# Kernel tuning notes

Hardware: AMD Instinct MI355X
Metric: run time of the kernel (lower is better)

Reference implementation:

```python
import jax, jax.numpy as jnp
import numpy as np
from functools import partial

S = 4096      # total tokens (single-request prefill)
H = 32        # indexer heads
D = 128       # indexer head dim (power of 2 for Hadamard)
R = 64        # rope head dim
QLR = 1536    # q_lora_rank
HID = 2048    # hidden size
TOPK = 2048   # index_topk
EPS = 1e-6
NEG = -1e30


def fwht(x):
    """Fast Walsh-Hadamard transform over last dim, scaled by d**-0.5."""
    d = x.shape[-1]
    orig = x.shape
    x = x.reshape(-1, d)
    h = 1
    while h < d:
        x = x.reshape(-1, d // (2 * h), 2, h)
        a, b = x[:, :, 0, :], x[:, :, 1, :]
        x = jnp.stack([a + b, a - b], axis=2).reshape(-1, d)
        h *= 2
    return (x * (d ** -0.5)).reshape(orig)


def apply_rope_interleaved(x, cos, sin):
    # non-neox (interleaved pairs): (x0,x1) -> (x0*c - x1*s, x0*s + x1*c)
    xe, xo = x[..., 0::2], x[..., 1::2]
    return jnp.stack([xe * cos - xo * sin, xe * sin + xo * cos], axis=-1).reshape(x.shape)


def setup_inputs() -> dict:
    key = jax.random.key(0)
    ks = jax.random.split(key, 8)
    hidden_states = jax.random.normal(ks[0], (S, HID), dtype=jnp.float32)
    q_lora = jax.random.normal(ks[1], (S, QLR), dtype=jnp.float32)
    positions = jnp.arange(S, dtype=jnp.int32)
    Wq = jax.random.normal(ks[2], (QLR, H * D), dtype=jnp.float32) * 0.02
    Wk = jax.random.normal(ks[3], (HID, D), dtype=jnp.float32) * 0.02
    k_gamma = jnp.ones((D,), dtype=jnp.float32)
    k_beta = jnp.zeros((D,), dtype=jnp.float32)
    Wp = jax.random.normal(ks[4], (HID, H), dtype=jnp.float32) * 0.02
    return {"hidden_states": hidden_states, "q_lora": q_lora, "positions": positions,
            "Wq": Wq, "Wk": Wk, "k_gamma": k_gamma, "k_beta": k_beta, "Wp": Wp}


def _indexer_logits(hidden_states, q_lora, Wq, Wk, k_gamma, k_beta, Wp, positions):
    # q projection: [S, QLR] @ [QLR, H*D] -> [S, H, D]
    q = (q_lora @ Wq).reshape(S, H, D)
    # k projection + layernorm: [S, D]
    k = hidden_states @ Wk
    mu = jnp.mean(k, axis=-1, keepdims=True)
    var = jnp.mean(jnp.square(k - mu), axis=-1, keepdims=True)
    k = (k - mu) * jax.lax.rsqrt(var + EPS) * k_gamma + k_beta
    # RoPE on first R dims (interleaved / non-neox style)
    half = R // 2
    inv_freq = 1.0 / (10000.0 ** (jnp.arange(half, dtype=jnp.float32) * 2.0 / R))
    ang = positions.astype(jnp.float32)[:, None] * inv_freq          # [S, half]
    cos, sin = jnp.cos(ang), jnp.sin(ang)
    q = q.at[..., :R].set(apply_rope_interleaved(q[..., :R], cos[:, None, :], sin[:, None, :]))
    k = k.at[..., :R].set(apply_rope_interleaved(k[..., :R], cos, sin))
    # Hadamard activation rotation
    q = fwht(q)
    k = fwht(k)
    # per-head gate: weights_proj(x) * n_heads^-0.5 * q_scale(=1) * softmax_scale
    w = (hidden_states @ Wp) * (H ** -0.5) * (D ** -0.5)             # [S, H]
    # logits[t, s] = sum_h w[t, h] * relu(q[t, h] . k[s]); scan over heads
    k_t = k.T                                                         # [D, S]
    def head_step(acc, inp):
        qh, wh = inp                                                  # [S, D], [S]
        return acc + wh[:, None] * jax.nn.relu(qh @ k_t), None
    logits, _ = jax.lax.scan(head_step, jnp.zeros((S, S), jnp.float32),
                             (q.transpose(1, 0, 2), w.T))
    # causal mask (ks=0, ke=t+1 per token for single-request prefill)
    idx = jnp.arange(S)
    logits = jnp.where(idx[None, :] <= idx[:, None], logits, NEG)
    return logits


def reference(hidden_states, q_lora, positions, Wq, Wk, k_gamma, k_beta, Wp):
    logits = _indexer_logits(hidden_states, q_lora, Wq, Wk, k_gamma, k_beta, Wp, positions)
    vals, topk_idx = jax.lax.top_k(logits, TOPK)                      # [S, TOPK]
    topk_idx = jnp.where(vals > NEG * 0.5, topk_idx, -1).astype(jnp.int32)
    return logits, topk_idx
```

## Files before the change

kernel.cpp:

```cpp
#include <hip/hip_runtime.h>
#include <hip/hip_bf16.h>
#include <math.h>

#define S 4096
#define H 32
#define D 128
#define QLR 1536
#define HID 2048
#define TOPK_N 2048
#define NEGF (-1e30f)
#define KW_N 160

typedef __attribute__((ext_vector_type(8))) short bf16x8;
typedef __attribute__((ext_vector_type(4))) float f32x4;

__device__ __forceinline__ void async_copy16(const void* g, void* l) {
    __builtin_amdgcn_global_load_lds(
        (const __attribute__((address_space(1))) unsigned int*)g,
        (__attribute__((address_space(3))) unsigned int*)l,
        16, 0, 0);
}

__device__ __forceinline__ unsigned short bf16bits(float f) {
    __hip_bfloat16 h = __float2bfloat16(f);
    return *(unsigned short*)&h;
}

__device__ __forceinline__ float bits2f(unsigned short u) {
    unsigned v = ((unsigned)u) << 16;
    return __uint_as_float(v);
}

__global__ __launch_bounds__(256) void cast_bf16_kernel(
    const float* __restrict__ in, __hip_bfloat16* __restrict__ out, int n4)
{
    int i = blockIdx.x * blockDim.x + threadIdx.x;
    if (i < n4) {
        float4 v = ((const float4*)in)[i];
        ushort4 pack;
        pack.x = bf16bits(v.x);
        pack.y = bf16bits(v.y);
        pack.z = bf16bits(v.z);
        pack.w = bf16bits(v.w);
        *(ushort4*)(out + (size_t)i * 4) = pack;
    }
}

__global__ __launch_bounds__(256) void zero_f32(float* __restrict__ p, int n)
{
    int i = blockIdx.x * blockDim.x + threadIdx.x;
    if (i < n) p[i] = 0.0f;
}

__global__ __launch_bounds__(256) void transpose_cast_kernel(
    const float* __restrict__ in, __hip_bfloat16* __restrict__ out)
{
    __shared__ float sm[32][33];
    const int nb = blockIdx.x;
    const int kb = blockIdx.y;
    const int t = threadIdx.x;
    const int j = t & 31, i0 = t >> 5;
#pragma unroll
    for (int u = 0; u < 4; ++u) {
        int i = i0 + u * 8;
        sm[i][j] = in[(size_t)(kb * 32 + i) * 4096 + nb * 32 + j];
    }
    __syncthreads();
#pragma unroll
    for (int u = 0; u < 4; ++u) {
        int i = i0 + u * 8;
        out[(size_t)(nb * 32 + i) * 1536 + kb * 32 + j] = __float2bfloat16(sm[j][i]);
    }
}

__global__ __launch_bounds__(256) void build_wkpT(
    const float* __restrict__ Wk, const float* __restrict__ Wp,
    __hip_bfloat16* __restrict__ WkpT)
{
    int g = blockIdx.x * blockDim.x + threadIdx.x;
    if (g >= KW_N * HID) return;
    int n = g / HID, k = g % HID;
    float v = (n < 128) ? Wk[(size_t)k * 128 + n]
                        : Wp[(size_t)k * 32 + (n - 128)] * 0.015625f;
    WkpT[g] = __float2bfloat16(v);
}

__device__ __forceinline__ void kw_stage(
    const short* __restrict__ hb, const short* __restrict__ WkpT,
    int mt, int koff, int rhi, int e, int wave, short* bufA, short* bufB)
{
#pragma unroll
    for (int it = 0; it < 4; ++it) {
        int r = it * 16 + rhi;
        async_copy16(hb + (size_t)(mt * 64 + r) * HID + koff + e * 8,
                     (void*)(bufA + it * 2048 + wave * 512));
    }
#pragma unroll
    for (int it = 0; it < 10; ++it) {
        int r = it * 16 + rhi;
        async_copy16(WkpT + (size_t)r * HID + koff + e * 8,
                     (void*)(bufB + it * 2048 + wave * 512));
    }
}

__global__ __launch_bounds__(256) void kw_mfma(
    const short* __restrict__ hb,
    const short* __restrict__ WkpT,
    float* __restrict__ kf32,
    float* __restrict__ wbuf)
{
    const int mt = blockIdx.x;
    const int kbase = blockIdx.y * 512;
    const int tid = threadIdx.x;
    const int wave = tid >> 6, lane = tid & 63, grp = lane >> 4, lm = lane & 15;
    __shared__ short As[2][64 * 128];
    __shared__ short Bs[2][KW_N * 128];

    const int rhi = tid >> 4;
    const int e = (tid & 15) ^ rhi;

    kw_stage(hb, WkpT, mt, kbase, rhi, e, wave, As[0], Bs[0]);

    f32x4 acc[10] = {};
    int cur = 0;
    for (int kc = 0; kc < 4; ++kc) {
        __syncthreads();
        if (kc < 3)
            kw_stage(hb, WkpT, mt, kbase + (kc + 1) * 128, rhi, e, wave,
                     As[cur ^ 1], Bs[cur ^ 1]);
#pragma unroll
        for (int k4 = 0; k4 < 4; ++k4) {
            int ch = ((k4 << 2) + grp) ^ lm;
            bf16x8 a = *(const bf16x8*)(As[cur] + (wave * 16 + lm) * 128 + ch * 8);
#pragma unroll
            for (int n = 0; n < 10; ++n) {
                bf16x8 b = *(const bf16x8*)(Bs[cur] + (n * 16 + lm) * 128 + ch * 8);
                acc[n] = __builtin_amdgcn_mfma_f32_16x16x32_bf16(a, b, acc[n], 0, 0, 0);
            }
        }
        cur ^= 1;
    }

#pragma unroll
    for (int n = 0; n < 10; ++n) {
#pragma unroll
        for (int r = 0; r < 4; ++r) {
            int row = mt * 64 + wave * 16 + grp * 4 + r;
            int col = n * 16 + lm;
            if (n < 8) atomicAdd(&kf32[(size_t)row * 128 + col], acc[n][r]);
            else       atomicAdd(&wbuf[(size_t)row * 32 + (col - 128)], acc[n][r]);
        }
    }
}

__device__ __forceinline__ void gemm_stage(
    const short* __restrict__ Ag, const short* __restrict__ Bg,
    int row0, int col0, int K, int kc, int tid, int wave, short* as, short* bs)
{
#pragma unroll
    for (int is = 0; is < 2; ++is) {
        int r = is * 64 + (tid >> 2);
        async_copy16(Ag + (size_t)(row0 + r) * K + kc + (tid & 3) * 8,
                     (void*)(as + is * 2048 + wave * 512));
        async_copy16(Bg + (size_t)(col0 + r) * K + kc + (tid & 3) * 8,
                     (void*)(bs + is * 2048 + wave * 512));
    }
}

__global__ __launch_bounds__(256, 2) void gemm_bf16_bt(
    const __hip_bfloat16* __restrict__ A, const __hip_bfloat16* __restrict__ BT,
    __hip_bfloat16* __restrict__ C, int M, int N, int K)
{
    __shared__ short As[2][128 * 32];
    __shared__ short Bs[2][128 * 32];
    const int tid = threadIdx.x;
    const int wave = tid >> 6, lane = tid & 63, grp = lane >> 4, lm = lane & 15;
    const int row0 = blockIdx.y * 128, col0 = blockIdx.x * 128;
    const short* Ag = (const short*)A;
    const short* Bg = (const short*)BT;

    f32x4 acc[2][8] = {};

    gemm_stage(Ag, Bg, row0, col0, K, 0, tid, wave, As[0], Bs[0]);
    int cur = 0;
    for (int kc = 0; kc < K; kc += 32) {
        __syncthreads();
        if (kc + 32 < K)
            gemm_stage(Ag, Bg, row0, col0, K, kc + 32, tid, wave,
                       As[cur ^ 1], Bs[cur ^ 1]);
        bf16x8 a0 = *(const bf16x8*)(As[cur] + (wave * 32 + lm) * 32 + grp * 8);
        bf16x8 a1 = *(const bf16x8*)(As[cur] + (wave * 32 + 16 + lm) * 32 + grp * 8);
#pragma unroll
        for (int c = 0; c < 8; ++c) {
            bf16x8 b = *(const bf16x8*)(Bs[cur] + (c * 16 + lm) * 32 + grp * 8);
            acc[0][c] = __builtin_amdgcn_mfma_f32_16x16x32_bf16(a0, b, acc[0][c], 0, 0, 0);
            acc[1][c] = __builtin_amdgcn_mfma_f32_16x16x32_bf16(a1, b, acc[1][c], 0, 0, 0);
        }
        cur ^= 1;
    }
#pragma unroll
    for (int t = 0; t < 2; ++t)
#pragma unroll
        for (int c = 0; c < 8; ++c)
#pragma unroll
            for (int r = 0; r < 4; ++r) {
                int rr = row0 + wave * 32 + t * 16 + grp * 4 + r;
                int cc = col0 + c * 16 + lm;
                C[(size_t)rr * N + cc] = __float2bfloat16(acc[t][c][r]);
            }
}

__global__ void sincos_table_kernel(const int* __restrict__ positions,
                                    float* __restrict__ cosT, float* __restrict__ sinT)
{
    int g = blockIdx.x * blockDim.x + threadIdx.x;
    if (g >= S * 32) return;
    int s = g >> 5;
    int p = g & 31;
    double inv = pow(10000.0, -((double)(2 * p)) / 64.0);
    double ang = (double)positions[s] * inv;
    cosT[g] = (float)cos(ang);
    sinT[g] = (float)sin(ang);
}

__global__ __launch_bounds__(256) void post_wave(
    const void* __restrict__ in, int in_bf16, __hip_bfloat16* __restrict__ outb,
    const float* __restrict__ cosT, const float* __restrict__ sinT,
    const float* __restrict__ gamma, const float* __restrict__ beta,
    int heads, int do_ln, int nrows)
{
    const int row = blockIdx.x * 4 + (threadIdx.x >> 6);
    if (row >= nrows) return;
    const int l = threadIdx.x & 63;
    const int srow = row / heads;

    float a, b;
    if (in_bf16) {
        unsigned pr = ((const unsigned*)in)[(size_t)row * 64 + l];
        a = bits2f((unsigned short)(pr & 0xffff));
        b = bits2f((unsigned short)(pr >> 16));
    } else {
        float2 v = ((const float2*)in)[(size_t)row * 64 + l];
        a = v.x; b = v.y;
    }

    if (do_ln) {
        float s = a + b;
#pragma unroll
        for (int o = 1; o < 64; o <<= 1) s += __shfl_xor(s, o);
        float mu = s * (1.0f / 128.0f);
        float da = a - mu, db = b - mu;
        float sq = da * da + db * db;
#pragma unroll
        for (int o = 1; o < 64; o <<= 1) sq += __shfl_xor(sq, o);
        float rs = rsqrtf(sq * (1.0f / 128.0f) + 1e-6f);
        float2 g = ((const float2*)gamma)[l];
        float2 bt = ((const float2*)beta)[l];
        a = da * rs * g.x + bt.x;
        b = db * rs * g.y + bt.y;
    }

    if (l < 32) {
        float c = cosT[(size_t)srow * 32 + l];
        float sn = sinT[(size_t)srow * 32 + l];
        float xe = a, xo = b;
        a = xe * c - xo * sn;
        b = xe * sn + xo * c;
    }

    {
        float na = a + b, nb = a - b;
        a = na; b = nb;
    }
#pragma unroll
    for (int m = 1; m < 64; m <<= 1) {
        float pa = __shfl_xor(a, m);
        float pb = __shfl_xor(b, m);
        if (l & m) { a = pa - a; b = pb - b; }
        else       { a = a + pa; b = b + pb; }
    }

    const float sc = 0.08838834764831845f;
    unsigned outp = (unsigned)bf16bits(a * sc) | ((unsigned)bf16bits(b * sc) << 16);
    ((unsigned*)outb)[(size_t)row * 64 + l] = outp;
}

__global__ __launch_bounds__(256, 3) void logits_mfma(
    const short* __restrict__ qb,
    const short* __restrict__ kb,
    const float* __restrict__ w,
    float* __restrict__ out)
{
    const int bx = blockIdx.x;
    const int by = blockIdx.y;
    const int row0 = by * 64, col0 = bx * 128;
    const int tid = threadIdx.x;

    if (2 * bx > by) {
        const float4 n4 = make_float4(NEGF, NEGF, NEGF, NEGF);
        int c = (tid & 31) * 4;
        for (int r = tid >> 5; r < 64; r += 8)
            *(float4*)&out[(size_t)(row0 + r) * S + col0 + c] = n4;
        return;
    }

    __shared__ short BsAs[128 * 128];
    __shared__ float Ws[64 * 33];

    const int wave = tid >> 6, lane = tid & 63, grp = lane >> 4, lm = lane & 15;
    const int wr = wave >> 1, wc = wave & 1;
    const int rhi = tid >> 4;
    const int e = (tid & 15) ^ rhi;

#pragma unroll
    for (int it = 0; it < 8; ++it) {
        int r = it * 16 + rhi;
        async_copy16(kb + (size_t)(col0 + r) * D + e * 8,
                     (void*)(BsAs + it * 2048 + wave * 512));
    }
    for (int i = tid; i < 64 * 32; i += 256) {
        int r = i >> 5, h = i & 31;
        Ws[r * 33 + h] = w[(size_t)row0 * H + i];
    }
    __syncthreads();

    bf16x8 bfrag[4][4];
#pragma unroll
    for (int c = 0; c < 4; ++c)
#pragma unroll
        for (int kc = 0; kc < 4; ++kc)
            bfrag[c][kc] = *(const bf16x8*)(
                BsAs + (wc * 64 + c * 16 + lm) * 128 + (((kc << 2) + grp) ^ lm) * 8);
    __syncthreads();

    short* As0 = BsAs;
    short* As1 = BsAs + 64 * 128;

#pragma unroll
    for (int it = 0; it < 4; ++it) {
        int r = it * 16 + rhi;
        async_copy16(qb + (size_t)(row0 + r) * (H * D) + e * 8,
                     (void*)(As0 + it * 2048 + wave * 512));
    }

    f32x4 accP[2][4] = {};

    for (int h = 0; h < H; ++h) {
        __syncthreads();
        short* Acur  = (h & 1) ? As1 : As0;
        short* Anext = (h & 1) ? As0 : As1;
        if (h + 1 < H) {
#pragma unroll
            for (int it = 0; it < 4; ++it) {
                int r = it * 16 + rhi;
                async_copy16(qb + (size_t)(row0 + r) * (H * D) + (h + 1) * D + e * 8,
                             (void*)(Anext + it * 2048 + wave * 512));
            }
        }
        float wv[2][4];
#pragma unroll
        for (int t = 0; t < 2; ++t)
#pragma unroll
            for (int r = 0; r < 4; ++r)
                wv[t][r] = Ws[(wr * 32 + t * 16 + grp * 4 + r) * 33 + h];

        f32x4 accH[2][4] = {};
        __builtin_amdgcn_s_setprio(1);
#pragma unroll
        for (int kc = 0; kc < 4; ++kc) {
            int ch = ((kc << 2) + grp) ^ lm;
            bf16x8 a0 = *(const bf16x8*)(Acur + (wr * 32 + lm) * 128 + ch * 8);
            bf16x8 a1 = *(const bf16x8*)(Acur + (wr * 32 + 16 + lm) * 128 + ch * 8);
#pragma unroll
            for (int c = 0; c < 4; ++c) {
                accH[0][c] = __builtin_amdgcn_mfma_f32_16x16x32_bf16(a0, bfrag[c][kc], accH[0][c], 0, 0, 0);
                accH[1][c] = __builtin_amdgcn_mfma_f32_16x16x32_bf16(a1, bfrag[c][kc], accH[1][c], 0, 0, 0);
            }
        }
        __builtin_amdgcn_s_setprio(0);
#pragma unroll
        for (int t = 0; t < 2; ++t)
#pragma unroll
            for (int c = 0; c < 4; ++c)
#pragma unroll
                for (int r = 0; r < 4; ++r)
                    accP[t][c][r] += wv[t][r] * fmaxf(accH[t][c][r], 0.0f);
    }

#pragma unroll
    for (int t = 0; t < 2; ++t)
#pragma unroll
        for (int c = 0; c < 4; ++c)
#pragma unroll
            for (int r = 0; r < 4; ++r) {
                int rr = row0 + wr * 32 + t * 16 + grp * 4 + r;
                int cc = col0 + wc * 64 + c * 16 + lm;
                out[(size_t)rr * S + cc] = (cc <= rr) ? accP[t][c][r] : NEGF;
            }
}

__device__ __forceinline__ unsigned mono32(float f)
{
    unsigned u = __float_as_uint(f);
    return (u & 0x80000000u) ? ~u : (u | 0x80000000u);
}

__global__ __launch_bounds__(256) void topk_select(
    const float* __restrict__ logits, float* __restrict__ out_idx)
{
    const int row = blockIdx.x;
    const int tid = threadIdx.x;
    const int valid = row + 1;
    float* orow = out_idx + (size_t)row * TOPK_N;

    if (valid <= TOPK_N) {
        for (int p = tid; p < TOPK_N; p += 256)
            orow[p] = (p < valid) ? (float)p : -1.0f;
        return;
    }

    __shared__ float vals[S];
    __shared__ unsigned hist[2048];
    __shared__ unsigned chunk[256];
    __shared__ unsigned long long sh_prefix;
    __shared__ int sh_rem;
    __shared__ unsigned sh_cnt;

    const float* lr = logits + (size_t)row * S;
    for (int j = tid; j < valid; j += 256) vals[j] = lr[j];
    if (tid == 0) { sh_prefix = 0ull; sh_rem = TOPK_N; sh_cnt = 0u; }
    __syncthreads();

    for (int rnd = 0; rnd < 4; ++rnd) {
        const int shift = 33 - 11 * rnd;
        for (int i = tid; i < 2048; i += 256) hist[i] = 0u;
        __syncthreads();
        const unsigned long long pref = sh_prefix;
        const int rem = sh_rem;
        const int hs = shift + 11;
        for (int j = tid; j < valid; j += 256) {
            unsigned long long key = (((unsigned long long)mono32(vals[j])) << 12)
                                   | (unsigned)(4095 - j);
            if ((key >> hs) == (pref >> hs))
                atomicAdd(&hist[(unsigned)(key >> shift) & 2047u], 1u);
        }
        __syncthreads();
        unsigned csum = 0;
#pragma unroll
        for (int d = 0; d < 8; ++d) csum += hist[tid * 8 + d];
        chunk[tid] = csum;
        __syncthreads();
        for (int off = 1; off < 256; off <<= 1) {
            unsigned v = (tid + off < 256) ? chunk[tid + off] : 0u;
            __syncthreads();
            chunk[tid] += v;
            __syncthreads();
        }
        unsigned A = (tid < 255) ? chunk[tid + 1] : 0u;
        for (int dd = 7; dd >= 0; --dd) {
            unsigned c = hist[tid * 8 + dd];
            if (c && A < (unsigned)rem && (unsigned)rem <= A + c) {
                sh_prefix = pref | ((unsigned long long)(tid * 8 + dd) << shift);
                sh_rem = rem - (int)A;
            }
            A += c;
        }
        __syncthreads();
    }

    const unsigned long long Kstar = sh_prefix;
    for (int j = tid; j < valid; j += 256) {
        unsigned long long key = (((unsigned long long)mono32(vals[j])) << 12)
                               | (unsigned)(4095 - j);
        if (key >= Kstar) {
            unsigned p = atomicAdd(&sh_cnt, 1u);
            orow[p] = (float)j;
        }
    }
}

extern "C" void kernel_launch(void* const* d_in, const int* in_sizes, int n_in,
                              void* d_out, int out_size, void* d_ws, size_t ws_size,
                              hipStream_t stream)
{
    const float* hidden    = (const float*)d_in[0];
    const float* q_lora    = (const float*)d_in[1];
    const int*   positions = (const int*)d_in[2];
    const float* Wq        = (const float*)d_in[3];
    const float* Wk        = (const float*)d_in[4];
    const float* k_gamma   = (const float*)d_in[5];
    const float* k_beta    = (const float*)d_in[6];
    const float* Wp        = (const float*)d_in[7];

    char* ws = (char*)d_ws;
    size_t off = 0;
    __hip_bfloat16* qb16 = (__hip_bfloat16*)(ws + off); off += (size_t)S * H * D * 2;
    __hip_bfloat16* qlb  = (__hip_bfloat16*)(ws + off); off += (size_t)S * QLR * 2;
    __hip_bfloat16* WqT  = (__hip_bfloat16*)(ws + off); off += (size_t)(H * D) * QLR * 2;
    __hip_bfloat16* hb   = (__hip_bfloat16*)(ws + off); off += (size_t)S * HID * 2;
    __hip_bfloat16* WkpT = (__hip_bfloat16*)(ws + off); off += (size_t)KW_N * HID * 2;
    float* kf32 = (float*)(ws + off); off += (size_t)S * D * 4;
    __hip_bfloat16* kb16 = (__hip_bfloat16*)(ws + off); off += (size_t)S * D * 2;
    float* wbuf = (float*)(ws + off); off += (size_t)S * H * 4;
    float* cosT = (float*)(ws + off); off += (size_t)S * 32 * 4;
    float* sinT = (float*)(ws + off); off += (size_t)S * 32 * 4;

    float* out_logits = (float*)d_out;
    float* out_idx = out_logits + (size_t)S * S;

    cast_bf16_kernel<<<(S * QLR / 4 + 255) / 256, 256, 0, stream>>>(q_lora, qlb, S * QLR / 4);
    transpose_cast_kernel<<<dim3((H * D) / 32, QLR / 32), 256, 0, stream>>>(Wq, WqT);

    gemm_bf16_bt<<<dim3((H * D) / 128, S / 128), 256, 0, stream>>>(
        qlb, WqT, qb16, S, H * D, QLR);

    cast_bf16_kernel<<<(S * HID / 4 + 255) / 256, 256, 0, stream>>>(hidden, hb, S * HID / 4);
    build_wkpT<<<(KW_N * HID + 255) / 256, 256, 0, stream>>>(Wk, Wp, WkpT);
    zero_f32<<<(S * D + 255) / 256, 256, 0, stream>>>(kf32, S * D);
    zero_f32<<<(S * H + 255) / 256, 256, 0, stream>>>(wbuf, S * H);
    kw_mfma<<<dim3(S / 64, 4), 256, 0, stream>>>(
        (const short*)hb, (const short*)WkpT, kf32, wbuf);

    sincos_table_kernel<<<(S * 32) / 256, 256, 0, stream>>>(positions, cosT, sinT);

    post_wave<<<(S + 3) / 4, 256, 0, stream>>>(
        kf32, 0, kb16, cosT, sinT, k_gamma, k_beta, 1, 1, S);
    post_wave<<<(S * H + 3) / 4, 256, 0, stream>>>(
        qb16, 1, qb16, cosT, sinT, nullptr, nullptr, H, 0, S * H);

    logits_mfma<<<dim3(S / 128, S / 64), 256, 0, stream>>>(
        (const short*)qb16, (const short*)kb16, wbuf, out_logits);

    topk_select<<<S, 256, 0, stream>>>(out_logits, out_idx);
}
```

Before: 437.9 us.

## Load Q fragments directly to registers in logits kernel, widen GEMM K-tile

The logits kernel no longer stages per-head Q tiles through LDS with barriers. Each wave now loads its Q fragments straight from global memory into registers, double-buffered across heads, so the per-head __syncthreads disappears. Occupancy is lowered to 2 blocks per CU to make room for the extra registers. The projection GEMM moves from a 32 to a 64-wide K tile with an XOR-swizzled LDS layout, and the sincos table uses float math instead of double, which may change numerics slightly.

```diff
diff --git a/kernel.cpp b/kernel.cpp
--- a/kernel.cpp
+++ b/kernel.cpp
@@ -153,17 +153,20 @@
     }
 }
 
-__device__ __forceinline__ void gemm_stage(
+__device__ __forceinline__ void gemm_stage64(
     const short* __restrict__ Ag, const short* __restrict__ Bg,
-    int row0, int col0, int K, int kc, int tid, int wave, short* as, short* bs)
-{
-#pragma unroll
-    for (int is = 0; is < 2; ++is) {
-        int r = is * 64 + (tid >> 2);
-        async_copy16(Ag + (size_t)(row0 + r) * K + kc + (tid & 3) * 8,
-                     (void*)(as + is * 2048 + wave * 512));
-        async_copy16(Bg + (size_t)(col0 + r) * K + kc + (tid & 3) * 8,
-                     (void*)(bs + is * 2048 + wave * 512));
+    int row0, int col0, int K, int kc, int tid, short* as, short* bs)
+{
+    const int w = tid >> 6, lane = tid & 63;
+    const int rsub = lane >> 3;
+    const int c = (lane & 7) ^ rsub;
+#pragma unroll
+    for (int i = 0; i < 4; ++i) {
+        int r = w * 32 + i * 8 + rsub;
+        async_copy16(Ag + (size_t)(row0 + r) * K + kc + c * 8,
+                     (void*)(as + (w * 32 + i * 8) * 64));
+        async_copy16(Bg + (size_t)(col0 + r) * K + kc + c * 8,
+                     (void*)(bs + (w * 32 + i * 8) * 64));
     }
 }
 
@@ -171,8 +174,8 @@
     const __hip_bfloat16* __restrict__ A, const __hip_bfloat16* __restrict__ BT,
     __hip_bfloat16* __restrict__ C, int M, int N, int K)
 {
-    __shared__ short As[2][128 * 32];
-    __shared__ short Bs[2][128 * 32];
+    __shared__ short As[2][128 * 64];
+    __shared__ short Bs[2][128 * 64];
     const int tid = threadIdx.x;
     const int wave = tid >> 6, lane = tid & 63, grp = lane >> 4, lm = lane & 15;
     const int row0 = blockIdx.y * 128, col0 = blockIdx.x * 128;
@@ -181,20 +184,24 @@
 
     f32x4 acc[2][8] = {};
 
-    gemm_stage(Ag, Bg, row0, col0, K, 0, tid, wave, As[0], Bs[0]);
+    gemm_stage64(Ag, Bg, row0, col0, K, 0, tid, As[0], Bs[0]);
     int cur = 0;
-    for (int kc = 0; kc < K; kc += 32) {
+    for (int kc = 0; kc < K; kc += 64) {
         __syncthreads();
-        if (kc + 32 < K)
-            gemm_stage(Ag, Bg, row0, col0, K, kc + 32, tid, wave,
-                       As[cur ^ 1], Bs[cur ^ 1]);
-        bf16x8 a0 = *(const bf16x8*)(As[cur] + (wave * 32 + lm) * 32 + grp * 8);
-        bf16x8 a1 = *(const bf16x8*)(As[cur] + (wave * 32 + 16 + lm) * 32 + grp * 8);
-#pragma unroll
-        for (int c = 0; c < 8; ++c) {
-            bf16x8 b = *(const bf16x8*)(Bs[cur] + (c * 16 + lm) * 32 + grp * 8);
-            acc[0][c] = __builtin_amdgcn_mfma_f32_16x16x32_bf16(a0, b, acc[0][c], 0, 0, 0);
-            acc[1][c] = __builtin_amdgcn_mfma_f32_16x16x32_bf16(a1, b, acc[1][c], 0, 0, 0);
+        if (kc + 64 < K)
+            gemm_stage64(Ag, Bg, row0, col0, K, kc + 64, tid,
+                         As[cur ^ 1], Bs[cur ^ 1]);
+#pragma unroll
+        for (int k2 = 0; k2 < 2; ++k2) {
+            int pos = ((k2 << 2) + grp) ^ (lm & 7);
+            bf16x8 a0 = *(const bf16x8*)(As[cur] + (wave * 32 + lm) * 64 + pos * 8);
+            bf16x8 a1 = *(const bf16x8*)(As[cur] + (wave * 32 + 16 + lm) * 64 + pos * 8);
+#pragma unroll
+            for (int c = 0; c < 8; ++c) {
+                bf16x8 b = *(const bf16x8*)(Bs[cur] + (c * 16 + lm) * 64 + pos * 8);
+                acc[0][c] = __builtin_amdgcn_mfma_f32_16x16x32_bf16(a0, b, acc[0][c], 0, 0, 0);
+                acc[1][c] = __builtin_amdgcn_mfma_f32_16x16x32_bf16(a1, b, acc[1][c], 0, 0, 0);
+            }
         }
         cur ^= 1;
     }
@@ -217,10 +224,12 @@
     if (g >= S * 32) return;
     int s = g >> 5;
     int p = g & 31;
-    double inv = pow(10000.0, -((double)(2 * p)) / 64.0);
-    double ang = (double)positions[s] * inv;
-    cosT[g] = (float)cos(ang);
-    sinT[g] = (float)sin(ang);
+    float inv = exp2f(-13.28771237954945f * (float)(2 * p) * (1.0f / 64.0f));
+    float ang = (float)positions[s] * inv;
+    float sv, cv;
+    sincosf(ang, &sv, &cv);
+    cosT[g] = cv;
+    sinT[g] = sv;
 }
 
 __global__ __launch_bounds__(256) void post_wave(
@@ -285,7 +294,7 @@
     ((unsigned*)outb)[(size_t)row * 64 + l] = outp;
 }
 
-__global__ __launch_bounds__(256, 3) void logits_mfma(
+__global__ __launch_bounds__(256, 2) void logits_mfma(
     const short* __restrict__ qb,
     const short* __restrict__ kb,
     const float* __restrict__ w,
@@ -304,7 +313,7 @@
         return;
     }
 
-    __shared__ short BsAs[128 * 128];
+    __shared__ short Bs[128 * 128];
     __shared__ float Ws[64 * 33];
 
     const int wave = tid >> 6, lane = tid & 63, grp = lane >> 4, lm = lane & 15;
@@ -316,7 +325,7 @@
     for (int it = 0; it < 8; ++it) {
         int r = it * 16 + rhi;
         async_copy16(kb + (size_t)(col0 + r) * D + e * 8,
-                     (void*)(BsAs + it * 2048 + wave * 512));
+                     (void*)(Bs + it * 2048 + wave * 512));
     }
     for (int i = tid; i < 64 * 32; i += 256) {
         int r = i >> 5, h = i & 31;
@@ -330,61 +339,50 @@
 #pragma unroll
         for (int kc = 0; kc < 4; ++kc)
             bfrag[c][kc] = *(const bf16x8*)(
-                BsAs + (wc * 64 + c * 16 + lm) * 128 + (((kc << 2) + grp) ^ lm) * 8);
-    __syncthreads();
-
-    short* As0 = BsAs;
-    short* As1 = BsAs + 64 * 128;
-
-#pragma unroll
-    for (int it = 0; it < 4; ++it) {
-        int r = it * 16 + rhi;
-        async_copy16(qb + (size_t)(row0 + r) * (H * D) + e * 8,
-                     (void*)(As0 + it * 2048 + wave * 512));
-    }
+                Bs + (wc * 64 + c * 16 + lm) * 128 + (((kc << 2) + grp) ^ lm) * 8);
+
+    const short* pa0 = qb + (size_t)(row0 + wr * 32 + lm) * (H * D) + grp * 8;
+    const short* pa1 = pa0 + (size_t)16 * (H * D);
 
     f32x4 accP[2][4] = {};
-
-    for (int h = 0; h < H; ++h) {
-        __syncthreads();
-        short* Acur  = (h & 1) ? As1 : As0;
-        short* Anext = (h & 1) ? As0 : As1;
-        if (h + 1 < H) {
-#pragma unroll
-            for (int it = 0; it < 4; ++it) {
-                int r = it * 16 + rhi;
-                async_copy16(qb + (size_t)(row0 + r) * (H * D) + (h + 1) * D + e * 8,
-                             (void*)(Anext + it * 2048 + wave * 512));
-            }
-        }
-        float wv[2][4];
-#pragma unroll
-        for (int t = 0; t < 2; ++t)
-#pragma unroll
-            for (int r = 0; r < 4; ++r)
-                wv[t][r] = Ws[(wr * 32 + t * 16 + grp * 4 + r) * 33 + h];
-
+    bf16x8 aA[2][4], aB[2][4];
+
+    auto loadA = [&](bf16x8 (&a)[2][4], int h) {
+#pragma unroll
+        for (int kc = 0; kc < 4; ++kc) {
+            a[0][kc] = *(const bf16x8*)(pa0 + h * 128 + kc * 32);
+            a[1][kc] = *(const bf16x8*)(pa1 + h * 128 + kc * 32);
+        }
+    };
+    auto computeH = [&](bf16x8 (&a)[2][4], int h) {
         f32x4 accH[2][4] = {};
         __builtin_amdgcn_s_setprio(1);
 #pragma unroll
         for (int kc = 0; kc < 4; ++kc) {
-            int ch = ((kc << 2) + grp) ^ lm;
-            bf16x8 a0 = *(const bf16x8*)(Acur + (wr * 32 + lm) * 128 + ch * 8);
-            bf16x8 a1 = *(const bf16x8*)(Acur + (wr * 32 + 16 + lm) * 128 + ch * 8);
 #pragma unroll
             for (int c = 0; c < 4; ++c) {
-                accH[0][c] = __builtin_amdgcn_mfma_f32_16x16x32_bf16(a0, bfrag[c][kc], accH[0][c], 0, 0, 0);
-                accH[1][c] = __builtin_amdgcn_mfma_f32_16x16x32_bf16(a1, bfrag[c][kc], accH[1][c], 0, 0, 0);
+                accH[0][c] = __builtin_amdgcn_mfma_f32_16x16x32_bf16(a[0][kc], bfrag[c][kc], accH[0][c], 0, 0, 0);
+                accH[1][c] = __builtin_amdgcn_mfma_f32_16x16x32_bf16(a[1][kc], bfrag[c][kc], accH[1][c], 0, 0, 0);
             }
         }
         __builtin_amdgcn_s_setprio(0);
 #pragma unroll
         for (int t = 0; t < 2; ++t)
 #pragma unroll
-            for (int c = 0; c < 4; ++c)
-#pragma unroll
-                for (int r = 0; r < 4; ++r)
-                    accP[t][c][r] += wv[t][r] * fmaxf(accH[t][c][r], 0.0f);
+            for (int r = 0; r < 4; ++r) {
+                float wv = Ws[(wr * 32 + t * 16 + grp * 4 + r) * 33 + h];
+#pragma unroll
+                for (int c = 0; c < 4; ++c)
+                    accP[t][c][r] += wv * fmaxf(accH[t][c][r], 0.0f);
+            }
+    };
+
+    loadA(aA, 0);
+    for (int h = 0; h < H; h += 2) {
+        loadA(aB, h + 1);
+        computeH(aA, h);
+        if (h + 2 < H) loadA(aA, h + 2);
+        computeH(aB, h + 1);
     }
 
 #pragma unroll
```

Measured after the change: 559.2 us. 1.28x slower.
